# Kernel tuning notes

Measured on AMD Instinct MI355X. Metric: run time of the kernel, lower is better.

The kernel has to match this reference:

```python
import jax, jax.numpy as jnp
import numpy as np

N_NODES = 100000
N_EDGES = 1600000
F_IN, F_HID, F_OUT = 15, 64, 64
N_MID = 6  # layers 1..6 of 8


def gcn_norm(edge_index, edge_weight, num_nodes):
    """PyG GCNConv normalization with self-loops (fill_value=1.0).
    Returns (src, dst, norm) over the augmented edge set."""
    src, dst = edge_index[0], edge_index[1]
    loop = jnp.arange(num_nodes)
    s = jnp.concatenate([src, loop])
    d = jnp.concatenate([dst, loop])
    w = jnp.concatenate([edge_weight, jnp.ones((num_nodes,), edge_weight.dtype)])
    deg = jax.ops.segment_sum(w, d, num_segments=num_nodes)
    dinv = jnp.where(deg > 0, jax.lax.rsqrt(deg), 0.0)
    norm = dinv[s] * w * dinv[d]  # [E+N]
    return s, d, norm


def gcn_layer(h, s, d, norm, W, b, num_nodes):
    h = h @ W                                  # dense transform [N, F_out]
    msg = norm[:, None] * h[s]                 # gather + scale   [E+N, F_out]
    out = jax.ops.segment_sum(msg, d, num_segments=num_nodes)  # scatter-add
    return out + b


def setup_inputs() -> dict:
    key = jax.random.key(0)
    ks = jax.random.split(key, 8)
    x = jax.random.normal(ks[0], (N_NODES, F_IN), jnp.float32)
    edge_index = jax.random.randint(ks[1], (2, N_EDGES), 0, N_NODES, jnp.int64)
    edge_weight = jax.random.uniform(ks[2], (N_EDGES,), jnp.float32)
    # glorot-ish scaling keeps activations sane through 8 layers
    W0 = jax.random.normal(ks[3], (F_IN, F_HID), jnp.float32) * (1.0 / np.sqrt(F_IN))
    b0 = jnp.zeros((F_HID,), jnp.float32)
    W_mid = jax.random.normal(ks[4], (N_MID, F_HID, F_HID), jnp.float32) * (1.0 / np.sqrt(F_HID))
    b_mid = jnp.zeros((N_MID, F_HID), jnp.float32)
    W_last = jax.random.normal(ks[5], (F_HID, F_OUT), jnp.float32) * (1.0 / np.sqrt(F_HID))
    b_last = jnp.zeros((F_OUT,), jnp.float32)
    return {"x": x, "edge_index": edge_index, "edge_weight": edge_weight,
            "W0": W0, "b0": b0, "W_mid": W_mid, "b_mid": b_mid,
            "W_last": W_last, "b_last": b_last}


def reference(x, edge_index, edge_weight, W0, b0, W_mid, b_mid, W_last, b_last):
    num_nodes = x.shape[0]
    s, d, norm = gcn_norm(edge_index, edge_weight, num_nodes)
    # layer 0
    h = gcn_layer(x, s, d, norm, W0, b0, num_nodes)
    h = jax.nn.relu(h)  # dropout is identity in eval mode
    # middle layers 1..6
    for i in range(N_MID):
        h = gcn_layer(h, s, d, norm, W_mid[i], b_mid[i], num_nodes)
        h = jax.nn.relu(h)
    # final layer + sigmoid
    h = gcn_layer(h, s, d, norm, W_last, b_last, num_nodes)
    return jax.nn.sigmoid(h)
```

## Files before the change

### kernel.cpp

```cpp
#include <hip/hip_runtime.h>
#include <hip/hip_fp16.h>
#include <math.h>

#define N_NODES 100000
#define N_EDGES 1600000
#define F_IN 15
#define NB_NODES 391
#define MASK40 ((1ull << 40) - 1)

typedef _Float16 half8 __attribute__((ext_vector_type(8)));
typedef float f32x4 __attribute__((ext_vector_type(4)));


__global__ void k_initp(unsigned long long* __restrict__ packed8) {
    int i = blockIdx.x * blockDim.x + threadIdx.x;
    if (i < 8 * N_NODES) packed8[i] = 0ull;
}

__global__ void k_cnt(const int* __restrict__ dst, const float* __restrict__ w,
                      unsigned long long* __restrict__ packed8, int* __restrict__ ord) {
    int i = blockIdx.x * blockDim.x + threadIdx.x;
    if (i >= N_EDGES) return;
    int copy = blockIdx.x & 7;
    int d = dst[i];
    unsigned long long contrib =
        (1ull << 40) + (unsigned long long)((double)w[i] * 4294967296.0);
    unsigned long long old = atomicAdd(&packed8[(size_t)copy * N_NODES + d], contrib);
    ord[i] = (int)(old >> 40);
}

__global__ void k_part(const unsigned long long* __restrict__ packed8,
                       int* __restrict__ bsum, float* __restrict__ dinv) {
    __shared__ int red[256];
    int t = threadIdx.x;
    int i = blockIdx.x * 256 + t;
    int c = 0;
    if (i < N_NODES) {
        unsigned long long wsum = 0;
#pragma unroll
        for (int cp = 0; cp < 8; cp++) {
            unsigned long long p = packed8[(size_t)cp * N_NODES + i];
            c += (int)(p >> 40);
            wsum += (p & MASK40);
        }
        float deg = 1.0f + (float)((double)wsum * 0x1p-32);
        dinv[i] = rsqrtf(deg);
    }
    red[t] = c;
    __syncthreads();
    for (int off = 128; off > 0; off >>= 1) {
        if (t < off) red[t] += red[t + off];
        __syncthreads();
    }
    if (t == 0) bsum[blockIdx.x] = red[0];
}

__global__ __launch_bounds__(512) void k_scanb(int* __restrict__ bsum,
                                               int* __restrict__ rowptr) {
    __shared__ int sc[512];
    int t = threadIdx.x;
    int v = (t < NB_NODES) ? bsum[t] : 0;
    sc[t] = v;
    __syncthreads();
    for (int off = 1; off < 512; off <<= 1) {
        int u = (t >= off) ? sc[t - off] : 0;
        __syncthreads();
        sc[t] += u;
        __syncthreads();
    }
    if (t < NB_NODES) bsum[t] = sc[t] - v;
    if (t == 0) rowptr[N_NODES] = N_EDGES;
}

__global__ void k_fillptr(const unsigned long long* __restrict__ packed8,
                          const int* __restrict__ bsum, int* __restrict__ rowptr,
                          int* __restrict__ rbase) {
    __shared__ int sc[256];
    int t = threadIdx.x;
    int i = blockIdx.x * 256 + t;
    int cnts[8];
    int v = 0;
    if (i < N_NODES) {
#pragma unroll
        for (int cp = 0; cp < 8; cp++) {
            cnts[cp] = (int)(packed8[(size_t)cp * N_NODES + i] >> 40);
            v += cnts[cp];
        }
    }
    sc[t] = v;
    __syncthreads();
    for (int off = 1; off < 256; off <<= 1) {
        int u = (t >= off) ? sc[t - off] : 0;
        __syncthreads();
        sc[t] += u;
        __syncthreads();
    }
    if (i < N_NODES) {
        int run = bsum[blockIdx.x] + sc[t] - v;
        rowptr[i] = run;
#pragma unroll
        for (int cp = 0; cp < 8; cp++) {
            rbase[(size_t)cp * N_NODES + i] = run;
            run += cnts[cp];
        }
    }
}

__global__ void k_fill(const int* __restrict__ src, const int* __restrict__ dst,
                       const float* __restrict__ w, const float* __restrict__ dinv,
                       const int* __restrict__ rbase, const int* __restrict__ ord,
                       int2* __restrict__ csr) {
    int i = blockIdx.x * blockDim.x + threadIdx.x;
    if (i >= N_EDGES) return;
    int copy = (i >> 8) & 7;
    int s = src[i], d = dst[i];
    float nm = dinv[s] * w[i] * dinv[d];
    csr[rbase[(size_t)copy * N_NODES + d] + ord[i]] = make_int2(s, __float_as_int(nm));
}


__global__ void k_gemm0(const float* __restrict__ x, const float* __restrict__ W,
                        __half* __restrict__ out) {
    __shared__ float Ws[F_IN * 64];
    int t = threadIdx.x;
    for (int i = t; i < F_IN * 64; i += 256) Ws[i] = W[i];
    __syncthreads();
    int r = blockIdx.x * 4 + (t >> 6);
    int c = t & 63;
    if (r < N_NODES) {
        const float* xr = x + (long)r * F_IN;
        float acc = 0.f;
#pragma unroll
        for (int k = 0; k < F_IN; k++) acc += xr[k] * Ws[k * 64 + c];
        out[(long)r * 64 + c] = __float2half(acc);
    }
}


#define SE_CAP 256
#define G_STRIDE 72

template <bool WEP, bool SIG>
__global__ __launch_bounds__(256) void k_gather4(
        const int* __restrict__ rowptr, const int2* __restrict__ csr,
        const __half* __restrict__ hin, const float* __restrict__ dinv,
        const float* __restrict__ W, const float* __restrict__ b,
        void* __restrict__ outp) {
    extern __shared__ char smem[];
    int t = threadIdx.x, wv = t >> 6, lane = t & 63;
    int sub = lane >> 5, fl = lane & 31;
    int2* se = (int2*)smem + wv * SE_CAP;
    _Float16* G = (_Float16*)(smem + 4 * SE_CAP * 8);

    int nb = blockIdx.x * 32;
    int n0w = nb + wv * 8;

    int rp[9];
#pragma unroll
    for (int j = 0; j < 9; j++) rp[j] = rowptr[n0w + j];
    int base = rp[0], end = rp[8];

    const __half2* h2 = (const __half2*)hin;

    float2 acc[8];
#pragma unroll
    for (int j = 0; j < 8; j++) {
        int n = n0w + j;
        float dv = dinv[n];
        float2 hf = __half22float2(h2[(long)n * 32 + fl]);
        float w0 = (sub == 0) ? dv * dv : 0.f;
        acc[j].x = w0 * hf.x;
        acc[j].y = w0 * hf.y;
    }

    for (int cb = base; cb < end; cb += SE_CAP) {
        int ce = cb + SE_CAP; if (ce > end) ce = end;
        int cn = ce - cb;
        for (int i = lane; i < cn; i += 64) se[i] = csr[cb + i];
        __builtin_amdgcn_wave_barrier();
#pragma unroll
        for (int j = 0; j < 8; j++) {
            int lo = rp[j] < cb ? cb : rp[j];
            int hi = rp[j + 1] > ce ? ce : rp[j + 1];
            int i = lo - cb, iend = hi - cb;
            for (; i + 7 < iend; i += 8) {
                int2 r0 = se[i + sub],     r1 = se[i + 2 + sub];
                int2 r2 = se[i + 4 + sub], r3 = se[i + 6 + sub];
                float2 f0 = __half22float2(h2[(long)r0.x * 32 + fl]);
                float2 f1 = __half22float2(h2[(long)r1.x * 32 + fl]);
                float2 f2 = __half22float2(h2[(long)r2.x * 32 + fl]);
                float2 f3 = __half22float2(h2[(long)r3.x * 32 + fl]);
                float n0 = __int_as_float(r0.y), n1 = __int_as_float(r1.y);
                float n2 = __int_as_float(r2.y), n3 = __int_as_float(r3.y);
                acc[j].x += n0 * f0.x; acc[j].y += n0 * f0.y;
                acc[j].x += n1 * f1.x; acc[j].y += n1 * f1.y;
                acc[j].x += n2 * f2.x; acc[j].y += n2 * f2.y;
                acc[j].x += n3 * f3.x; acc[j].y += n3 * f3.y;
            }
            for (; i + 1 < iend; i += 2) {
                int2 r = se[i + sub];
                float2 f = __half22float2(h2[(long)r.x * 32 + fl]);
                float nm = __int_as_float(r.y);
                acc[j].x += nm * f.x; acc[j].y += nm * f.y;
            }
            if (i < iend) {
                int2 r = se[i];
                float2 f = __half22float2(h2[(long)r.x * 32 + fl]);
                float nm = (sub == 0) ? __int_as_float(r.y) : 0.f;
                acc[j].x += nm * f.x; acc[j].y += nm * f.y;
            }
        }
        __builtin_amdgcn_wave_barrier();
    }

#pragma unroll
    for (int j = 0; j < 8; j++) {
        acc[j].x += __shfl_xor(acc[j].x, 32);
        acc[j].y += __shfl_xor(acc[j].y, 32);
    }

    if (!WEP) {
        float2 bv = ((const float2*)b)[fl];
        if (sub == 0) {
#pragma unroll
            for (int j = 0; j < 8; j++) {
                float ox = fmaxf(acc[j].x + bv.x, 0.f);
                float oy = fmaxf(acc[j].y + bv.y, 0.f);
                ((__half2*)outp)[(long)(n0w + j) * 32 + fl] = __floats2half2_rn(ox, oy);
            }
        }
        return;
    }

    if (sub == 0) {
        __half2* G2 = (__half2*)G;
#pragma unroll
        for (int j = 0; j < 8; j++)
            G2[(wv * 8 + j) * (G_STRIDE / 2) + fl] = __floats2half2_rn(acc[j].x, acc[j].y);
    }
    __syncthreads();

    int col = lane & 15, quad = lane >> 4;
    int mrow = (wv & 1) * 16;
    int nc0 = (wv >> 1) * 32;

    half8 af[2];
#pragma unroll
    for (int kt = 0; kt < 2; kt++)
        af[kt] = *(const half8*)&G[(mrow + col) * G_STRIDE + kt * 32 + quad * 8];

    half8 bf[2][2][2];
#pragma unroll
    for (int nt = 0; nt < 2; nt++) {
#pragma unroll
        for (int kt = 0; kt < 2; kt++) {
#pragma unroll
            for (int j = 0; j < 8; j++) {
                float w = W[(kt * 32 + quad * 8 + j) * 64 + nc0 + nt * 16 + col];
                _Float16 hi = (_Float16)w;
                bf[nt][kt][0][j] = hi;
                bf[nt][kt][1][j] = (_Float16)(w - (float)hi);
            }
        }
    }

    f32x4 c0, c1;
    {
        float b0v = b[nc0 + col], b1v = b[nc0 + 16 + col];
        c0 = (f32x4){b0v, b0v, b0v, b0v};
        c1 = (f32x4){b1v, b1v, b1v, b1v};
    }
#pragma unroll
    for (int kt = 0; kt < 2; kt++) {
        c0 = __builtin_amdgcn_mfma_f32_16x16x32_f16(af[kt], bf[0][kt][0], c0, 0, 0, 0);
        c0 = __builtin_amdgcn_mfma_f32_16x16x32_f16(af[kt], bf[0][kt][1], c0, 0, 0, 0);
        c1 = __builtin_amdgcn_mfma_f32_16x16x32_f16(af[kt], bf[1][kt][0], c1, 0, 0, 0);
        c1 = __builtin_amdgcn_mfma_f32_16x16x32_f16(af[kt], bf[1][kt][1], c1, 0, 0, 0);
    }

#pragma unroll
    for (int nt = 0; nt < 2; nt++) {
        f32x4 c = nt ? c1 : c0;
#pragma unroll
        for (int r = 0; r < 4; r++) {
            long node = nb + mrow + quad * 4 + r;
            int feat = nc0 + nt * 16 + col;
            float o = c[r];
            if (SIG) {
                o = 1.0f / (1.0f + expf(-o));
                ((float*)outp)[node * 64 + feat] = o;
            } else {
                o = fmaxf(o, 0.f);
                ((__half*)outp)[node * 64 + feat] = __float2half(o);
            }
        }
    }
}


extern "C" void kernel_launch(void* const* d_in, const int* in_sizes, int n_in,
                              void* d_out, int out_size, void* d_ws, size_t ws_size,
                              hipStream_t stream) {
    const float* x  = (const float*)d_in[0];
    const int*   ei = (const int*)  d_in[1];
    const float* ew = (const float*)d_in[2];
    const float* W0 = (const float*)d_in[3];
    const float* b0 = (const float*)d_in[4];
    const float* Wm = (const float*)d_in[5];
    const float* bm = (const float*)d_in[6];
    const float* Wl = (const float*)d_in[7];
    const float* bl = (const float*)d_in[8];
    float* out = (float*)d_out;

    const int* src = ei;
    const int* dst = ei + N_EDGES;

    char* ws = (char*)d_ws;
    unsigned long long* packed8 = (unsigned long long*)(ws + 0);
    float*  dinv   = (float*)(ws + (7u  << 20));
    int*    rowptr = (int*)  (ws + (8u  << 20));
    int*    bsum   = (int*)  (ws + (9u  << 20));
    int*    ord    = (int*)  (ws + (9u  << 20) + 65536);
    int*    rbase  = (int*)  (ws + (16u << 20));
    int2*   csr    = (int2*) (ws + (20u << 20));
    __half* htmp   = (__half*)(ws + (33u << 20));
    __half* hA     = (__half*)(ws + (46u << 20));
    __half* hB     = (__half*)(ws + (59u << 20));

    const int BT = 256;
    dim3 blk(BT);
    int gN  = NB_NODES;
    int gN8 = (8 * N_NODES + BT - 1) / BT;
    int gE  = (N_EDGES + BT - 1) / BT;
    int gR4 = (N_NODES + 3) / 4;
    int gG  = N_NODES / 32;

    const size_t smem0 = 4 * SE_CAP * 8;
    const size_t smemW = 4 * SE_CAP * 8 + 32 * G_STRIDE * 2;

    hipLaunchKernelGGL(k_initp,   dim3(gN8), blk, 0, stream, packed8);
    hipLaunchKernelGGL(k_cnt,     dim3(gE),  blk, 0, stream, dst, ew, packed8, ord);
    hipLaunchKernelGGL(k_part,    dim3(gN),  blk, 0, stream, packed8, bsum, dinv);
    hipLaunchKernelGGL(k_scanb,   dim3(1), dim3(512), 0, stream, bsum, rowptr);
    hipLaunchKernelGGL(k_fillptr, dim3(gN),  blk, 0, stream, packed8, bsum, rowptr, rbase);
    hipLaunchKernelGGL(k_fill,    dim3(gE),  blk, 0, stream, src, dst, ew, dinv, rbase, ord, csr);

    hipLaunchKernelGGL(k_gemm0,   dim3(gR4), blk, 0, stream, x, W0, htmp);
    hipLaunchKernelGGL((k_gather4<false, false>), dim3(gG), blk, smem0, stream,
                       rowptr, csr, htmp, dinv, (const float*)nullptr, b0, (void*)hA);

    __half* hin = hA;
    __half* hout = hB;
    for (int i = 0; i < 6; i++) {
        const float* Wi = Wm + (long)i * 64 * 64;
        const float* bi = bm + (long)i * 64;
        hipLaunchKernelGGL((k_gather4<true, false>), dim3(gG), blk, smemW, stream,
                           rowptr, csr, hin, dinv, Wi, bi, (void*)hout);
        __half* t2 = hin; hin = hout; hout = t2;
    }

    hipLaunchKernelGGL((k_gather4<true, true>), dim3(gG), blk, smemW, stream,
                       rowptr, csr, hin, dinv, Wl, bl, (void*)out);
}
```

Measured before the change: 562.5 us.

## Build CSR via two-level bucket sort instead of global atomic counting

Replaces the global-atomic CSR construction (8-way replicated packed counters, per-edge ordinal, scattered fill) with a bucketed counting sort. Edges are first histogrammed and scattered into 512-node destination buckets using shared-memory atomics. Each bucket is then processed in shared memory to compute degrees, row pointers and the final CSR placement. This aims to cut global atomic contention and random global writes in the preprocessing phase. It adds an intermediate edge buffer, packs the source index into 17 bits, and relies on N_EDGES dividing evenly across the 256 blocks.

```diff
diff --git a/kernel.cpp b/kernel.cpp
--- a/kernel.cpp
+++ b/kernel.cpp
@@ -5,62 +5,101 @@
 #define N_NODES 100000
 #define N_EDGES 1600000
 #define F_IN 15
-#define NB_NODES 391
 #define MASK40 ((1ull << 40) - 1)
+
+#define NBLK1 256
+#define EPB   (N_EDGES / NBLK1)
+#define NBUCK 256
+#define NBUCK_USED ((N_NODES + 511) >> 9)
 
 typedef _Float16 half8 __attribute__((ext_vector_type(8)));
 typedef float f32x4 __attribute__((ext_vector_type(4)));
 
 
-__global__ void k_initp(unsigned long long* __restrict__ packed8) {
-    int i = blockIdx.x * blockDim.x + threadIdx.x;
-    if (i < 8 * N_NODES) packed8[i] = 0ull;
-}
-
-__global__ void k_cnt(const int* __restrict__ dst, const float* __restrict__ w,
-                      unsigned long long* __restrict__ packed8, int* __restrict__ ord) {
-    int i = blockIdx.x * blockDim.x + threadIdx.x;
-    if (i >= N_EDGES) return;
-    int copy = blockIdx.x & 7;
-    int d = dst[i];
-    unsigned long long contrib =
-        (1ull << 40) + (unsigned long long)((double)w[i] * 4294967296.0);
-    unsigned long long old = atomicAdd(&packed8[(size_t)copy * N_NODES + d], contrib);
-    ord[i] = (int)(old >> 40);
-}
-
-__global__ void k_part(const unsigned long long* __restrict__ packed8,
-                       int* __restrict__ bsum, float* __restrict__ dinv) {
-    __shared__ int red[256];
+__global__ __launch_bounds__(1024) void k_hist(const int* __restrict__ dst,
+                                               int* __restrict__ hist) {
+    __shared__ int bins[NBUCK];
+    int t = threadIdx.x, blk = blockIdx.x;
+    if (t < NBUCK) bins[t] = 0;
+    __syncthreads();
+    int e0 = blk * EPB;
+    for (int e = e0 + t; e < e0 + EPB; e += 1024)
+        atomicAdd(&bins[dst[e] >> 9], 1);
+    __syncthreads();
+    if (t < NBUCK) hist[t * NBLK1 + blk] = bins[t];
+}
+
+__global__ __launch_bounds__(1024) void k_scan(int* __restrict__ hist,
+                                               int* __restrict__ bucketBase,
+                                               int* __restrict__ rowptr) {
+    __shared__ int sc[1024];
     int t = threadIdx.x;
-    int i = blockIdx.x * 256 + t;
-    int c = 0;
-    if (i < N_NODES) {
-        unsigned long long wsum = 0;
-#pragma unroll
-        for (int cp = 0; cp < 8; cp++) {
-            unsigned long long p = packed8[(size_t)cp * N_NODES + i];
-            c += (int)(p >> 40);
-            wsum += (p & MASK40);
-        }
-        float deg = 1.0f + (float)((double)wsum * 0x1p-32);
-        dinv[i] = rsqrtf(deg);
-    }
-    red[t] = c;
-    __syncthreads();
-    for (int off = 128; off > 0; off >>= 1) {
-        if (t < off) red[t] += red[t + off];
+    int base = t * 64;
+    int vals[64];
+    int tot = 0;
+#pragma unroll
+    for (int k = 0; k < 64; k++) { vals[k] = hist[base + k]; tot += vals[k]; }
+    sc[t] = tot;
+    __syncthreads();
+    for (int off = 1; off < 1024; off <<= 1) {
+        int u = (t >= off) ? sc[t - off] : 0;
         __syncthreads();
-    }
-    if (t == 0) bsum[blockIdx.x] = red[0];
-}
-
-__global__ __launch_bounds__(512) void k_scanb(int* __restrict__ bsum,
-                                               int* __restrict__ rowptr) {
+        sc[t] += u;
+        __syncthreads();
+    }
+    int run = sc[t] - tot;
+#pragma unroll
+    for (int k = 0; k < 64; k++) {
+        int idx = base + k;
+        if ((idx & (NBLK1 - 1)) == 0) bucketBase[idx / NBLK1] = run;
+        int v = vals[k];
+        hist[idx] = run;
+        run += v;
+    }
+    if (t == 0) { bucketBase[NBUCK] = N_EDGES; rowptr[N_NODES] = N_EDGES; }
+}
+
+__global__ __launch_bounds__(1024) void k_scatter(const int* __restrict__ src,
+        const int* __restrict__ dst, const float* __restrict__ w,
+        const int* __restrict__ hist, int2* __restrict__ brec) {
+    __shared__ int cursor[NBUCK];
+    int t = threadIdx.x, blk = blockIdx.x;
+    if (t < NBUCK) cursor[t] = hist[t * NBLK1 + blk];
+    __syncthreads();
+    int e0 = blk * EPB;
+    for (int e = e0 + t; e < e0 + EPB; e += 1024) {
+        int d = dst[e];
+        int pos = atomicAdd(&cursor[d >> 9], 1);
+        brec[pos] = make_int2(src[e] | ((d & 511) << 17), __float_as_int(w[e]));
+    }
+}
+
+__global__ __launch_bounds__(512) void k_deg(const int2* __restrict__ brec,
+        const int* __restrict__ bucketBase, float* __restrict__ dinv,
+        int* __restrict__ rowptr) {
+    __shared__ unsigned long long packedl[512];
     __shared__ int sc[512];
-    int t = threadIdx.x;
-    int v = (t < NB_NODES) ? bsum[t] : 0;
-    sc[t] = v;
+    int t = threadIdx.x, b = blockIdx.x;
+    packedl[t] = 0ull;
+    __syncthreads();
+    int ebase = bucketBase[b], eend = bucketBase[b + 1];
+    for (int e = ebase + t; e < eend; e += 512) {
+        int2 r = brec[e];
+        int dlo = (r.x >> 17) & 511;
+        float wv = __int_as_float(r.y);
+        unsigned long long contrib =
+            (1ull << 40) + (unsigned long long)((double)wv * 4294967296.0);
+        atomicAdd(&packedl[dlo], contrib);
+    }
+    __syncthreads();
+    unsigned long long p = packedl[t];
+    int cnt = (int)(p >> 40);
+    int n = (b << 9) + t;
+    if (n < N_NODES) {
+        float deg = 1.0f + (float)((double)(p & MASK40) * 0x1p-32);
+        dinv[n] = rsqrtf(deg);
+    }
+    sc[t] = cnt;
     __syncthreads();
     for (int off = 1; off < 512; off <<= 1) {
         int u = (t >= off) ? sc[t - off] : 0;
@@ -68,54 +107,29 @@
         sc[t] += u;
         __syncthreads();
     }
-    if (t < NB_NODES) bsum[t] = sc[t] - v;
-    if (t == 0) rowptr[N_NODES] = N_EDGES;
-}
-
-__global__ void k_fillptr(const unsigned long long* __restrict__ packed8,
-                          const int* __restrict__ bsum, int* __restrict__ rowptr,
-                          int* __restrict__ rbase) {
-    __shared__ int sc[256];
-    int t = threadIdx.x;
-    int i = blockIdx.x * 256 + t;
-    int cnts[8];
-    int v = 0;
-    if (i < N_NODES) {
-#pragma unroll
-        for (int cp = 0; cp < 8; cp++) {
-            cnts[cp] = (int)(packed8[(size_t)cp * N_NODES + i] >> 40);
-            v += cnts[cp];
-        }
-    }
-    sc[t] = v;
-    __syncthreads();
-    for (int off = 1; off < 256; off <<= 1) {
-        int u = (t >= off) ? sc[t - off] : 0;
-        __syncthreads();
-        sc[t] += u;
-        __syncthreads();
-    }
-    if (i < N_NODES) {
-        int run = bsum[blockIdx.x] + sc[t] - v;
-        rowptr[i] = run;
-#pragma unroll
-        for (int cp = 0; cp < 8; cp++) {
-            rbase[(size_t)cp * N_NODES + i] = run;
-            run += cnts[cp];
-        }
-    }
-}
-
-__global__ void k_fill(const int* __restrict__ src, const int* __restrict__ dst,
-                       const float* __restrict__ w, const float* __restrict__ dinv,
-                       const int* __restrict__ rbase, const int* __restrict__ ord,
-                       int2* __restrict__ csr) {
-    int i = blockIdx.x * blockDim.x + threadIdx.x;
-    if (i >= N_EDGES) return;
-    int copy = (i >> 8) & 7;
-    int s = src[i], d = dst[i];
-    float nm = dinv[s] * w[i] * dinv[d];
-    csr[rbase[(size_t)copy * N_NODES + d] + ord[i]] = make_int2(s, __float_as_int(nm));
+    if (n < N_NODES) rowptr[n] = ebase + sc[t] - cnt;
+}
+
+__global__ __launch_bounds__(512) void k_csr(const int2* __restrict__ brec,
+        const int* __restrict__ bucketBase, const int* __restrict__ rowptr,
+        const float* __restrict__ dinv, int2* __restrict__ csr) {
+    __shared__ int cursor[512];
+    __shared__ float dl[512];
+    int t = threadIdx.x, b = blockIdx.x;
+    int n = (b << 9) + t;
+    if (n < N_NODES) { cursor[t] = rowptr[n]; dl[t] = dinv[n]; }
+    else             { cursor[t] = 0;         dl[t] = 0.f; }
+    __syncthreads();
+    int ebase = bucketBase[b], eend = bucketBase[b + 1];
+    for (int e = ebase + t; e < eend; e += 512) {
+        int2 r = brec[e];
+        int dlo = (r.x >> 17) & 511;
+        int s = r.x & 0x1FFFF;
+        float wv = __int_as_float(r.y);
+        int slot = atomicAdd(&cursor[dlo], 1);
+        float nm = dinv[s] * wv * dl[dlo];
+        csr[slot] = make_int2(s, __float_as_int(nm));
+    }
 }
 
 
@@ -316,37 +330,30 @@
     const int* dst = ei + N_EDGES;
 
     char* ws = (char*)d_ws;
-    unsigned long long* packed8 = (unsigned long long*)(ws + 0);
-    float*  dinv   = (float*)(ws + (7u  << 20));
-    int*    rowptr = (int*)  (ws + (8u  << 20));
-    int*    bsum   = (int*)  (ws + (9u  << 20));
-    int*    ord    = (int*)  (ws + (9u  << 20) + 65536);
-    int*    rbase  = (int*)  (ws + (16u << 20));
-    int2*   csr    = (int2*) (ws + (20u << 20));
-    __half* htmp   = (__half*)(ws + (33u << 20));
-    __half* hA     = (__half*)(ws + (46u << 20));
-    __half* hB     = (__half*)(ws + (59u << 20));
-
-    const int BT = 256;
-    dim3 blk(BT);
-    int gN  = NB_NODES;
-    int gN8 = (8 * N_NODES + BT - 1) / BT;
-    int gE  = (N_EDGES + BT - 1) / BT;
+    int*    hist   = (int*)  (ws + 0);
+    int*    bbase  = (int*)  (ws + (1u << 18));
+    float*  dinv   = (float*)(ws + (1u << 20));
+    int*    rowptr = (int*)  (ws + (2u << 20));
+    int2*   brec   = (int2*) (ws + (3u << 20));
+    int2*   csr    = (int2*) (ws + (16u << 20));
+    __half* htmp   = (__half*)(ws + (29u << 20));
+    __half* hA     = (__half*)(ws + (42u << 20));
+    __half* hB     = (__half*)(ws + (55u << 20));
+
     int gR4 = (N_NODES + 3) / 4;
     int gG  = N_NODES / 32;
 
     const size_t smem0 = 4 * SE_CAP * 8;
     const size_t smemW = 4 * SE_CAP * 8 + 32 * G_STRIDE * 2;
 
-    hipLaunchKernelGGL(k_initp,   dim3(gN8), blk, 0, stream, packed8);
-    hipLaunchKernelGGL(k_cnt,     dim3(gE),  blk, 0, stream, dst, ew, packed8, ord);
-    hipLaunchKernelGGL(k_part,    dim3(gN),  blk, 0, stream, packed8, bsum, dinv);
-    hipLaunchKernelGGL(k_scanb,   dim3(1), dim3(512), 0, stream, bsum, rowptr);
-    hipLaunchKernelGGL(k_fillptr, dim3(gN),  blk, 0, stream, packed8, bsum, rowptr, rbase);
-    hipLaunchKernelGGL(k_fill,    dim3(gE),  blk, 0, stream, src, dst, ew, dinv, rbase, ord, csr);
-
-    hipLaunchKernelGGL(k_gemm0,   dim3(gR4), blk, 0, stream, x, W0, htmp);
-    hipLaunchKernelGGL((k_gather4<false, false>), dim3(gG), blk, smem0, stream,
+    hipLaunchKernelGGL(k_hist,    dim3(NBLK1), dim3(1024), 0, stream, dst, hist);
+    hipLaunchKernelGGL(k_scan,    dim3(1),     dim3(1024), 0, stream, hist, bbase, rowptr);
+    hipLaunchKernelGGL(k_scatter, dim3(NBLK1), dim3(1024), 0, stream, src, dst, ew, hist, brec);
+    hipLaunchKernelGGL(k_deg,     dim3(NBUCK_USED), dim3(512), 0, stream, brec, bbase, dinv, rowptr);
+    hipLaunchKernelGGL(k_csr,     dim3(NBUCK_USED), dim3(512), 0, stream, brec, bbase, rowptr, dinv, csr);
+
+    hipLaunchKernelGGL(k_gemm0,   dim3(gR4), dim3(256), 0, stream, x, W0, htmp);
+    hipLaunchKernelGGL((k_gather4<false, false>), dim3(gG), dim3(256), smem0, stream,
                        rowptr, csr, htmp, dinv, (const float*)nullptr, b0, (void*)hA);
 
     __half* hin = hA;
@@ -354,11 +361,11 @@
     for (int i = 0; i < 6; i++) {
         const float* Wi = Wm + (long)i * 64 * 64;
         const float* bi = bm + (long)i * 64;
-        hipLaunchKernelGGL((k_gather4<true, false>), dim3(gG), blk, smemW, stream,
+        hipLaunchKernelGGL((k_gather4<true, false>), dim3(gG), dim3(256), smemW, stream,
                            rowptr, csr, hin, dinv, Wi, bi, (void*)hout);
         __half* t2 = hin; hin = hout; hout = t2;
     }
 
-    hipLaunchKernelGGL((k_gather4<true, true>), dim3(gG), blk, smemW, stream,
+    hipLaunchKernelGGL((k_gather4<true, true>), dim3(gG), dim3(256), smemW, stream,
                        rowptr, csr, hin, dinv, Wl, bl, (void*)out);
 }
```

After: 505.6 us. 10.1% less time.
